# Kernel tuning notes

Measured on AMD Instinct MI355X. Metric: run time of the kernel, lower is better.

The kernel has to match this reference:

```python
import jax, jax.numpy as jnp
import numpy as np

ALPHA = 0.1       # args.alpha
T = 1.0           # args.T temperature
SIGMA = 64.0      # Gaussian kernel bandwidth of kernel_function
B_CONST = 1.0     # B in get_lambda
N_ITERS = 50      # 2^-50 << tol=1e-8, matches the break condition of the 1000-iter loop
HW = 256          # image resolution (upsample target)


def _features(feat):
    # get_feature: bilinear upsample (align_corners=False == half-pixel, as jax.image.resize) then sigmoid(x/T)
    n, c, _, _ = feat.shape
    up = jax.image.resize(feat, (n, c, HW, HW), method='bilinear')
    return jax.nn.sigmoid(up / T)


def setup_inputs() -> dict:
    key = jax.random.key(0)
    k1, k2, k3, k4 = jax.random.split(key, 4)
    return {
        'cal_feat': jax.random.normal(k1, (256, 1, 64, 64), jnp.float32),
        'test_feat': jax.random.normal(k2, (32, 1, 64, 64), jnp.float32),
        'cal_gt': jax.random.randint(k3, (256, 1, 256, 256), 0, 2, jnp.int32),
        'test_gt': jax.random.randint(k4, (32, 1, 256, 256), 0, 2, jnp.int32),
    }


def reference(cal_feat, test_feat, cal_gt, test_gt):
    cal_res = _features(cal_feat)    # [N,1,H,W] in (0,1)
    test_res = _features(test_feat)  # [B,1,H,W]
    N = cal_res.shape[0]
    B = test_res.shape[0]
    f32 = cal_res.dtype

    # kernel_function.get_weight: Gaussian RBF on flattened features, plus self-weight 1, row-normalized -> [B, N+1]
    cf = cal_res.reshape(N, -1)
    tf = test_res.reshape(B, -1)
    d2 = (tf * tf).sum(-1)[:, None] + (cf * cf).sum(-1)[None, :] - 2.0 * (tf @ cf.T)
    k = jnp.exp(-d2 / (2.0 * SIGMA * SIGMA))
    w = jnp.concatenate([k, jnp.ones((B, 1), f32)], axis=1)
    w = w / w.sum(axis=1, keepdims=True)

    # FNR_i(t) = #{positive pixels of cal sample i with score < t} / #positives
    # (pred = res >= t, so false negatives are positive pixels with res < t). Precompute sorted
    # positive-pixel scores per cal sample so the bisection is a batched searchsorted.
    gt = (cal_gt > 0).reshape(N, -1)
    pos = jnp.sum(gt, axis=1)                                    # [N]
    scores = jnp.where(gt, cal_res.reshape(N, -1), jnp.inf)
    sorted_scores = jnp.sort(scores, axis=1)                     # [N, HW*HW], padding at +inf
    pos_f = jnp.maximum(pos, 1).astype(f32)

    def fnr_at(t):  # t: [B] thresholds -> [N, B]
        cnt = jax.vmap(lambda s: jnp.searchsorted(s, t, side='left'))(sorted_scores)
        return cnt.astype(f32) / pos_f[:, None]

    # batched bisection on lambda (get_lambda, vectorized over the B test samples)
    def body(carry, _):
        low, high = carry
        lam = 0.5 * (low + high)
        fnr = fnr_at(1.0 - lam)                                   # [N, B]
        risk = jnp.einsum('bn,nb->b', w[:, :-1], fnr) + w[:, -1] * B_CONST
        high = jnp.where(risk < ALPHA, lam, high)
        low = jnp.where(risk >= ALPHA, lam, low)
        return (low, high), None

    init = (jnp.zeros((B,), f32), jnp.ones((B,), f32))
    (low, _), _ = jax.lax.scan(body, init, None, length=N_ITERS)
    lam = low  # _lambda = low after the loop

    # prediction set, size and per-test FNR (get_fnr_list on the test sample)
    pred = test_res >= (1.0 - lam)[:, None, None, None]           # [B,1,H,W] bool
    size = jnp.sum(pred, axis=(1, 2, 3)).astype(f32)
    tgt = test_gt > 0
    tp = jnp.sum(pred & tgt, axis=(1, 2, 3)).astype(f32)
    tpos = jnp.maximum(jnp.sum(tgt, axis=(1, 2, 3)), 1).astype(f32)
    fnr_test = 1.0 - tp / tpos                                    # fdr_tensor, [B]
    return fnr_test, lam, size
```

## Files before the change

kernel.cpp:

```cpp
#include <hip/hip_runtime.h>


#define NPIX 65536
#define HB 16256
#define CDF_STRIDE 16272
#define ALPHA 0.1f

#define OFF_TESTRES  0
#define OFF_CALBF    8388608u
#define OFF_TESTBF   41943040u
#define OFF_GROUPED  46137344u
#define OFF_CDF      79691776u
#define OFF_GPART    96354304u
#define OFF_CC       98451456u
#define OFF_TT       98452480u
#define OFF_THR      98452608u
#define OFF_LAM      98452736u
#define OFF_FACC     98452864u

typedef __attribute__((ext_vector_type(8))) short bf16x8;
typedef __attribute__((ext_vector_type(16))) float f32x16;

__device__ __forceinline__ unsigned short f2bf_rne(float f) {
  unsigned u = __float_as_uint(f);
  return (unsigned short)((u + 0x7FFFu + ((u >> 16) & 1u)) >> 16);
}

__device__ __forceinline__ int hsl(int b) { return b ^ ((b >> 6) & 31); }

__device__ __forceinline__ float score_at(const float* __restrict__ sfeat,
                                          int x0, int x1, float wx, int y) {
  float sy = 0.25f * (float)y - 0.375f;
  int y0 = (int)floorf(sy);
  float wy = sy - (float)y0;
  int y1 = y0 + 1;
  if (y0 < 0) y0 = 0;
  if (y1 > 63) y1 = 63;
  float a = sfeat[y0 * 64 + x0] * (1.f - wx) + sfeat[y0 * 64 + x1] * wx;
  float b = sfeat[y1 * 64 + x0] * (1.f - wx) + sfeat[y1 * 64 + x1] * wx;
  float v = a * (1.f - wy) + b * wy;
  return 1.f / (1.f + __expf(-v));
}

__global__ __launch_bounds__(1024, 4) void k_calt(const float* __restrict__ featc,
                                                  const int* __restrict__ gt,
                                                  unsigned short* __restrict__ calbf,
                                                  unsigned* __restrict__ cdf,
                                                  unsigned short* __restrict__ grouped,
                                                  float* __restrict__ cc,
                                                  const float* __restrict__ featt,
                                                  float* __restrict__ tres,
                                                  unsigned short* __restrict__ tbf) {
  __shared__ unsigned smem[16704];
  __shared__ float sfeat[4096];
  __shared__ float tfeat[4096];
  const int tid = threadIdx.x;
  const int lane = tid & 63, wv = tid >> 6;
  const int x = tid & 255, yq = tid >> 8;
  float sx = 0.25f * (float)x - 0.375f;
  int x0 = (int)floorf(sx);
  float wx = sx - (float)x0;
  int x1 = x0 + 1;
  if (x0 < 0) x0 = 0;
  if (x1 > 63) x1 = 63;

  const int n = blockIdx.x;
  const int b = n >> 3, sl = n & 7;
  for (int i = tid; i < HB; i += 1024) smem[i] = 0;
  for (int i = tid; i < 4096; i += 1024) {
    sfeat[i] = featc[n * 4096 + i];
    tfeat[i] = featt[b * 4096 + i];
  }
  const int* gtn = gt + (size_t)n * NPIX;
  unsigned short* cbn = calbf + (size_t)n * NPIX;
  __syncthreads();

  {
    float* resb = tres + (size_t)b * NPIX + sl * 8192;
    unsigned short* tbn = tbf + (size_t)b * NPIX + sl * 8192;
    #pragma unroll
    for (int i = 0; i < 8; ++i) {
      int y = sl * 32 + i * 4 + yq;
      float s = score_at(tfeat, x0, x1, wx, y);
      int q = i * 1024 + tid;
      resb[q] = s;
      tbn[q] = f2bf_rne(s);
    }
  }

  unsigned long long pm = 0ull;
  float sumsq = 0.f;
  #pragma unroll 4
  for (int it = 0; it < 64; ++it) {
    int y = it * 4 + yq;
    float s = score_at(sfeat, x0, x1, wx, y);
    int p = (y << 8) + x;
    unsigned short bh = f2bf_rne(s);
    cbn[p] = bh;
    float sr = __uint_as_float((unsigned)bh << 16);
    sumsq += sr * sr;
    if (gtn[p] > 0) {
      pm |= (1ull << it);
      atomicAdd(&smem[hsl((int)(__float_as_uint(s) >> 16))], 1u);
    }
  }
  #pragma unroll
  for (int off = 32; off; off >>= 1) sumsq += __shfl_xor(sumsq, off);
  if (lane == 0) smem[16272 + wv] = __float_as_uint(sumsq);
  __syncthreads();
  if (tid == 0) {
    float c = 0.f;
    for (int w = 0; w < 16; ++w) c += __uint_as_float(smem[16272 + w]);
    cc[n] = c;
  }
  unsigned* cdfn = cdf + (size_t)n * CDF_STRIDE;
  if (tid < 256) {
    const int base = tid * 64;
    unsigned psum = 0;
    if (base < HB) {
      for (int j = 0; j < 64; ++j) psum += smem[hsl(base + j)];
    }
    unsigned inc = psum;
    #pragma unroll
    for (int off = 1; off < 64; off <<= 1) {
      unsigned v = __shfl_up(inc, off);
      if (lane >= off) inc += v;
    }
    if (lane == 63) smem[16256 + wv] = inc;
    smem[16320 + tid] = inc - psum;
  }
  __syncthreads();
  if (tid < 256) {
    unsigned woff = 0;
    for (int w = 0; w < wv; ++w) woff += smem[16256 + w];
    unsigned run = woff + smem[16320 + tid];
    const int base = tid * 64;
    if (base < HB) {
      for (int j = 0; j < 64; ++j) {
        int sj = hsl(base + j);
        unsigned hcnt = smem[sj];
        cdfn[base + j] = run;
        smem[sj] = run;
        run += hcnt;
      }
    }
    if (tid == 0)
      cdfn[HB] = smem[16256] + smem[16257] + smem[16258] + smem[16259];
  }
  __syncthreads();
  unsigned short* gn = grouped + (size_t)n * NPIX;
  for (int it = 0; it < 64; ++it) {
    if (pm & (1ull << it)) {
      int y = it * 4 + yq;
      float s = score_at(sfeat, x0, x1, wx, y);
      unsigned bits = __float_as_uint(s);
      unsigned idx = atomicAdd(&smem[hsl((int)(bits >> 16))], 1u);
      gn[idx] = (unsigned short)(bits & 0xFFFFu);
    }
  }
}

__global__ __launch_bounds__(1024) void k_tt(const unsigned short* __restrict__ tbf,
                                             float* __restrict__ tt) {
  __shared__ unsigned smem[16];
  const int tid = threadIdx.x;
  const int lane = tid & 63, wv = tid >> 6;
  const int x = tid & 255, yq = tid >> 8;
  const int b = blockIdx.x;
  const unsigned short* tbn = tbf + (size_t)b * NPIX;
  float sumsq = 0.f;
  #pragma unroll 4
  for (int it = 0; it < 64; ++it) {
    int p = ((it * 4 + yq) << 8) + x;
    float sr = __uint_as_float((unsigned)tbn[p] << 16);
    sumsq += sr * sr;
  }
  #pragma unroll
  for (int off = 32; off; off >>= 1) sumsq += __shfl_xor(sumsq, off);
  if (lane == 0) smem[wv] = __float_as_uint(sumsq);
  __syncthreads();
  if (tid == 0) {
    float t = 0.f;
    for (int w = 0; w < 16; ++w) t += __uint_as_float(smem[w]);
    tt[b] = t;
  }
}

__global__ __launch_bounds__(256) void k_gemm(const unsigned short* __restrict__ tbf,
                                              const unsigned short* __restrict__ cbf,
                                              float* __restrict__ gpart) {
  __shared__ __align__(16) unsigned short As[16384];
  __shared__ __align__(16) unsigned short Bs[16384];
  __shared__ float lred[4][1024];
  const int tid = threadIdx.x;
  const int lane = tid & 63, wv = tid >> 6;
  const int r = lane & 31, half = lane >> 5;
  const int nt = blockIdx.x;
  f32x16 acc;
  #pragma unroll
  for (int i = 0; i < 16; ++i) acc[i] = 0.f;
  for (int ch = 0; ch < 2; ++ch) {
    const size_t kbase = (size_t)blockIdx.y * 1024 + ch * 512;
    __syncthreads();
    #pragma unroll
    for (int s = 0; s < 16; ++s) {
      int flat = s * 256 + tid;
      int rem = flat & 2047;
      int row = rem >> 6, kb = rem & 63;
      const unsigned short* src = (flat >= 2048)
          ? cbf + (size_t)(nt * 32 + row) * NPIX + kbase + kb * 8
          : tbf + (size_t)row * NPIX + kbase + kb * 8;
      int slot = ((kb << 5) + row) ^ (kb & 31);
      int4 v = *(const int4*)src;
      *(int4*)((flat >= 2048 ? Bs : As) + slot * 8) = v;
    }
    __syncthreads();
    #pragma unroll
    for (int i = 0; i < 8; ++i) {
      int k8 = (wv << 4) + i * 2 + half;
      int slot = ((k8 << 5) + r) ^ (k8 & 31);
      bf16x8 a = *(const bf16x8*)(As + slot * 8);
      bf16x8 b = *(const bf16x8*)(Bs + slot * 8);
      acc = __builtin_amdgcn_mfma_f32_32x32x16_bf16(a, b, acc, 0, 0, 0);
    }
  }
  #pragma unroll
  for (int rg = 0; rg < 16; ++rg) {
    int m = (rg & 3) + 8 * (rg >> 2) + 4 * half;
    lred[wv][m * 32 + r] = acc[rg];
  }
  __syncthreads();
  float* gp = gpart + (size_t)(blockIdx.y * 8 + nt) * 1024;
  for (int e = tid; e < 1024; e += 256)
    gp[e] = lred[0][e] + lred[1][e] + lred[2][e] + lred[3][e];
}

__global__ __launch_bounds__(512) void k_quant(const float* __restrict__ gpart,
                                               const float* __restrict__ cc,
                                               const float* __restrict__ tt,
                                               const unsigned* __restrict__ cdf,
                                               const unsigned short* __restrict__ grouped,
                                               float* __restrict__ lam,
                                               float* __restrict__ thr,
                                               int* __restrict__ facc) {
  __shared__ float qs[256];
  __shared__ float bins[4096];
  __shared__ float red[8];
  __shared__ float bc[2];
  __shared__ unsigned sBin;
  const int b = blockIdx.x, tid = threadIdx.x;
  const int lane = tid & 63, wv = tid >> 6;

  if (tid < 4) facc[b * 4 + tid] = 0;
  for (int i = tid; i < 4096; i += 512) bins[i] = 0.f;
  if (tid == 0) sBin = 0xFFFFFFFFu;

  float k = 0.f;
  if (tid < 256) {
    const float* gp = gpart + ((tid >> 5) * 1024) + (b * 32) + (tid & 31);
    float g = 0.f;
    #pragma unroll 8
    for (int ks = 0; ks < 64; ++ks) g += gp[(size_t)ks * 8192];
    float d2 = tt[b] + cc[tid] - 2.f * g;
    k = expf(-d2 * (1.f / 8192.f));
  }
  float v = k;
  #pragma unroll
  for (int off = 32; off; off >>= 1) v += __shfl_xor(v, off);
  if (lane == 0) red[wv] = v;
  __syncthreads();
  if (tid == 0) {
    float ws = 1.f;
    for (int w = 0; w < 8; ++w) ws += red[w];
    bc[0] = ws;
  }
  __syncthreads();
  const float wsum = bc[0];
  const float wlast = 1.f / wsum;
  const float R = ALPHA - wlast;
  if (R <= 0.f) {
    if (tid == 0) { lam[b] = 1.0f; thr[b] = 0.0f; }
    return;
  }
  if (tid < 256) {
    unsigned pos = cdf[(size_t)tid * CDF_STRIDE + HB];
    qs[tid] = k / (wsum * (float)(pos ? pos : 1u));
  }
  __syncthreads();

  int lo = 0, hi = HB;
  float baseS = 0.f;
  for (int it = 0; it < 14; ++it) {
    int mid = (lo + hi) >> 1;
    float p = 0.f;
    if (tid < 256) p = qs[tid] * (float)cdf[(size_t)tid * CDF_STRIDE + mid];
    float r = p;
    #pragma unroll
    for (int off = 32; off; off >>= 1) r += __shfl_xor(r, off);
    if (lane == 0) red[wv] = r;
    __syncthreads();
    if (tid == 0) {
      float s = 0.f;
      for (int w = 0; w < 8; ++w) s += red[w];
      bc[1] = s;
    }
    __syncthreads();
    float S = bc[1];
    if (S < R) { lo = mid; baseS = S; } else { hi = mid; }
  }
  const int B = lo;

  {
    const int n = tid >> 1;
    const float q = qs[n];
    const unsigned* cn = cdf + (size_t)n * CDF_STRIDE;
    const unsigned short* gn = grouped + (size_t)n * NPIX;
    unsigned e0 = cn[B + 1];
    for (unsigned j = cn[B] + (tid & 1); j < e0; j += 2)
      atomicAdd(&bins[gn[j] >> 4], q);
  }
  __syncthreads();

  if (wv == 0) {
    float s = 0.f;
    for (int j = 0; j < 64; ++j) s += bins[lane * 64 + j];
    float inc = s;
    #pragma unroll
    for (int off = 1; off < 64; off <<= 1) {
      float u = __shfl_up(inc, off);
      if (lane >= off) inc += u;
    }
    float pre = inc - s;
    bool hit = (baseS + pre < R) && (baseS + inc >= R);
    unsigned long long m = __ballot(hit);
    int ow = m ? (__ffsll((unsigned long long)m) - 1) : -1;
    if (lane == ow) {
      float run = baseS + pre;
      unsigned bin = (unsigned)lane * 64 + 63;
      for (int j = 0; j < 64; ++j) {
        float bv = bins[lane * 64 + j];
        if (run + bv >= R) { bin = (unsigned)lane * 64 + j; break; }
        run += bv;
      }
      sBin = bin;
    }
    if (m == 0 && lane == 0) sBin = 4095u;
  }
  __syncthreads();
  if (tid == 0) {
    unsigned tb = ((unsigned)B << 16) | (sBin << 4);
    lam[b] = 1.0f - __uint_as_float(tb | 0x8u);
    thr[b] = __uint_as_float((tb | 0xFu) + 1u);
  }
}

__global__ __launch_bounds__(256) void k_finalp(const float* __restrict__ tres,
                                                const int* __restrict__ tgt,
                                                const float* __restrict__ thr,
                                                int* __restrict__ facc) {
  __shared__ int red[12];
  const int b = blockIdx.x, seg = blockIdx.y, tid = threadIdx.x;
  const int lane = tid & 63, wv = tid >> 6;
  const float th = thr[b];
  const float* rb = tres + (size_t)b * NPIX + seg * 8192;
  const int* gb = tgt + (size_t)b * NPIX + seg * 8192;
  int sz = 0, tp = 0, tpos = 0;
  for (int i = 0; i < 32; ++i) {
    int p = i * 256 + tid;
    int pred = (rb[p] >= th) ? 1 : 0;
    int tg = (gb[p] > 0) ? 1 : 0;
    sz += pred;
    tp += pred & tg;
    tpos += tg;
  }
  #pragma unroll
  for (int off = 32; off; off >>= 1) {
    sz += __shfl_xor(sz, off);
    tp += __shfl_xor(tp, off);
    tpos += __shfl_xor(tpos, off);
  }
  if (lane == 0) { red[wv] = sz; red[4 + wv] = tp; red[8 + wv] = tpos; }
  __syncthreads();
  if (tid == 0) {
    int s0 = red[0] + red[1] + red[2] + red[3];
    int s1 = red[4] + red[5] + red[6] + red[7];
    int s2 = red[8] + red[9] + red[10] + red[11];
    atomicAdd(&facc[b * 4 + 0], s0);
    atomicAdd(&facc[b * 4 + 1], s1);
    atomicAdd(&facc[b * 4 + 2], s2);
  }
}

__global__ void k_out(const int* __restrict__ facc, const float* __restrict__ lam,
                      float* __restrict__ out) {
  int b = threadIdx.x;
  if (b < 32) {
    int sz = facc[b * 4], tp = facc[b * 4 + 1], tpos = facc[b * 4 + 2];
    float tposf = (float)(tpos > 0 ? tpos : 1);
    out[b] = 1.f - (float)tp / tposf;
    out[32 + b] = lam[b];
    out[64 + b] = (float)sz;
  }
}

extern "C" void kernel_launch(void* const* d_in, const int* in_sizes, int n_in,
                              void* d_out, int out_size, void* d_ws, size_t ws_size,
                              hipStream_t stream) {
  const float* cal_feat = (const float*)d_in[0];
  const float* test_feat = (const float*)d_in[1];
  const int* cal_gt = (const int*)d_in[2];
  const int* test_gt = (const int*)d_in[3];
  float* out = (float*)d_out;
  char* ws = (char*)d_ws;

  float* test_res = (float*)(ws + OFF_TESTRES);
  unsigned short* cal_bf = (unsigned short*)(ws + OFF_CALBF);
  unsigned short* test_bf = (unsigned short*)(ws + OFF_TESTBF);
  unsigned short* grouped = (unsigned short*)(ws + OFF_GROUPED);
  unsigned* cdf = (unsigned*)(ws + OFF_CDF);
  float* gpart = (float*)(ws + OFF_GPART);
  float* cc = (float*)(ws + OFF_CC);
  float* tt = (float*)(ws + OFF_TT);
  float* thr = (float*)(ws + OFF_THR);
  float* lam = (float*)(ws + OFF_LAM);
  int* facc = (int*)(ws + OFF_FACC);

  k_calt<<<dim3(256), dim3(1024), 0, stream>>>(cal_feat, cal_gt, cal_bf, cdf, grouped, cc,
                                               test_feat, test_res, test_bf);
  k_tt<<<dim3(32), dim3(1024), 0, stream>>>(test_bf, tt);
  k_gemm<<<dim3(8, 64), dim3(256), 0, stream>>>(test_bf, cal_bf, gpart);
  k_quant<<<dim3(32), dim3(512), 0, stream>>>(gpart, cc, tt, cdf, grouped, lam, thr, facc);
  k_finalp<<<dim3(32, 8), dim3(256), 0, stream>>>(test_res, test_gt, thr, facc);
  k_out<<<dim3(1), dim3(64), 0, stream>>>(facc, lam, out);
}
```

Measured before the change: 255.3 us.

## Pack histogram into 16-bit pairs, stage grouped scatter in LDS, vectorize final pass

Packs two adjacent 16-bit histogram bins into each 32-bit LDS word, halving histogram memory. The prefix scan now uses all 1024 threads instead of 256. The freed LDS holds a staging buffer, so the bucketed scatter of positive scores goes to shared memory and is then written to global memory contiguously instead of as random global stores. The final prediction kernel reads float4/int4 vectors. The trade-off is much higher LDS use per block (launch bound drops from 4 to 2 blocks), and 16-bit packed counts could overflow if a bin pair ever exceeds 65535.

```diff
diff --git a/kernel.cpp b/kernel.cpp
--- a/kernel.cpp
+++ b/kernel.cpp
@@ -5,6 +5,7 @@
 #define HB 16256
 #define CDF_STRIDE 16272
 #define ALPHA 0.1f
+#define STAGE_CAP 40960
 
 #define OFF_TESTRES  0
 #define OFF_CALBF    8388608u
@@ -26,7 +27,7 @@
   return (unsigned short)((u + 0x7FFFu + ((u >> 16) & 1u)) >> 16);
 }
 
-__device__ __forceinline__ int hsl(int b) { return b ^ ((b >> 6) & 31); }
+__device__ __forceinline__ int SW(int w) { return w ^ ((w >> 5) & 31); }
 
 __device__ __forceinline__ float score_at(const float* __restrict__ sfeat,
                                           int x0, int x1, float wx, int y) {
@@ -42,7 +43,7 @@
   return 1.f / (1.f + __expf(-v));
 }
 
-__global__ __launch_bounds__(1024, 4) void k_calt(const float* __restrict__ featc,
+__global__ __launch_bounds__(1024, 2) void k_calt(const float* __restrict__ featc,
                                                   const int* __restrict__ gt,
                                                   unsigned short* __restrict__ calbf,
                                                   unsigned* __restrict__ cdf,
@@ -51,9 +52,10 @@
                                                   const float* __restrict__ featt,
                                                   float* __restrict__ tres,
                                                   unsigned short* __restrict__ tbf) {
-  __shared__ unsigned smem[16704];
+  __shared__ unsigned smem[9264];
   __shared__ float sfeat[4096];
   __shared__ float tfeat[4096];
+  __shared__ unsigned short sstage[STAGE_CAP];
   const int tid = threadIdx.x;
   const int lane = tid & 63, wv = tid >> 6;
   const int x = tid & 255, yq = tid >> 8;
@@ -66,7 +68,7 @@
 
   const int n = blockIdx.x;
   const int b = n >> 3, sl = n & 7;
-  for (int i = tid; i < HB; i += 1024) smem[i] = 0;
+  for (int i = tid; i < 8192; i += 1024) smem[i] = 0;
   for (int i = tid; i < 4096; i += 1024) {
     sfeat[i] = featc[n * 4096 + i];
     tfeat[i] = featt[b * 4096 + i];
@@ -90,7 +92,7 @@
 
   unsigned long long pm = 0ull;
   float sumsq = 0.f;
-  #pragma unroll 4
+  #pragma unroll 8
   for (int it = 0; it < 64; ++it) {
     int y = it * 4 + yq;
     float s = score_at(sfeat, x0, x1, wx, y);
@@ -101,52 +103,59 @@
     sumsq += sr * sr;
     if (gtn[p] > 0) {
       pm |= (1ull << it);
-      atomicAdd(&smem[hsl((int)(__float_as_uint(s) >> 16))], 1u);
+      unsigned bits = __float_as_uint(s);
+      atomicAdd(&smem[SW((int)(bits >> 17))], (bits & 0x10000u) ? 0x10000u : 1u);
     }
   }
   #pragma unroll
   for (int off = 32; off; off >>= 1) sumsq += __shfl_xor(sumsq, off);
-  if (lane == 0) smem[16272 + wv] = __float_as_uint(sumsq);
+  if (lane == 0) smem[8208 + wv] = __float_as_uint(sumsq);
   __syncthreads();
   if (tid == 0) {
     float c = 0.f;
-    for (int w = 0; w < 16; ++w) c += __uint_as_float(smem[16272 + w]);
+    for (int w = 0; w < 16; ++w) c += __uint_as_float(smem[8208 + w]);
     cc[n] = c;
   }
+  const int wbase = tid * 8;
+  unsigned psum = 0;
+  #pragma unroll
+  for (int j = 0; j < 8; ++j) {
+    unsigned w = smem[SW(wbase + j)];
+    psum += (w & 0xFFFFu) + (w >> 16);
+  }
+  unsigned inc = psum;
+  #pragma unroll
+  for (int off = 1; off < 64; off <<= 1) {
+    unsigned v = __shfl_up(inc, off);
+    if (lane >= off) inc += v;
+  }
+  if (lane == 63) smem[8192 + wv] = inc;
+  smem[8224 + tid] = inc - psum;
+  __syncthreads();
+  {
+    unsigned woff = 0;
+    for (int w = 0; w < wv; ++w) woff += smem[8192 + w];
+    unsigned run = woff + smem[8224 + tid];
+    #pragma unroll
+    for (int j = 0; j < 8; ++j) {
+      int si = SW(wbase + j);
+      unsigned w = smem[si];
+      unsigned clo = run;
+      run += (w & 0xFFFFu);
+      unsigned chi = run;
+      run += (w >> 16);
+      smem[si] = (chi << 16) | clo;
+    }
+    if (tid == 1023) smem[9248] = run;
+  }
+  __syncthreads();
   unsigned* cdfn = cdf + (size_t)n * CDF_STRIDE;
-  if (tid < 256) {
-    const int base = tid * 64;
-    unsigned psum = 0;
-    if (base < HB) {
-      for (int j = 0; j < 64; ++j) psum += smem[hsl(base + j)];
-    }
-    unsigned inc = psum;
-    #pragma unroll
-    for (int off = 1; off < 64; off <<= 1) {
-      unsigned v = __shfl_up(inc, off);
-      if (lane >= off) inc += v;
-    }
-    if (lane == 63) smem[16256 + wv] = inc;
-    smem[16320 + tid] = inc - psum;
-  }
-  __syncthreads();
-  if (tid < 256) {
-    unsigned woff = 0;
-    for (int w = 0; w < wv; ++w) woff += smem[16256 + w];
-    unsigned run = woff + smem[16320 + tid];
-    const int base = tid * 64;
-    if (base < HB) {
-      for (int j = 0; j < 64; ++j) {
-        int sj = hsl(base + j);
-        unsigned hcnt = smem[sj];
-        cdfn[base + j] = run;
-        smem[sj] = run;
-        run += hcnt;
-      }
-    }
-    if (tid == 0)
-      cdfn[HB] = smem[16256] + smem[16257] + smem[16258] + smem[16259];
-  }
+  for (int i = tid; i < HB; i += 1024) {
+    unsigned w = smem[SW(i >> 1)];
+    cdfn[i] = (i & 1) ? (w >> 16) : (w & 0xFFFFu);
+  }
+  const unsigned pos = smem[9248];
+  if (tid == 0) cdfn[HB] = pos;
   __syncthreads();
   unsigned short* gn = grouped + (size_t)n * NPIX;
   for (int it = 0; it < 64; ++it) {
@@ -154,10 +163,16 @@
       int y = it * 4 + yq;
       float s = score_at(sfeat, x0, x1, wx, y);
       unsigned bits = __float_as_uint(s);
-      unsigned idx = atomicAdd(&smem[hsl((int)(bits >> 16))], 1u);
-      gn[idx] = (unsigned short)(bits & 0xFFFFu);
-    }
-  }
+      unsigned old = atomicAdd(&smem[SW((int)(bits >> 17))], (bits & 0x10000u) ? 0x10000u : 1u);
+      unsigned idx = (bits & 0x10000u) ? (old >> 16) : (old & 0xFFFFu);
+      unsigned short lo = (unsigned short)(bits & 0xFFFFu);
+      if (idx < STAGE_CAP) sstage[idx] = lo;
+      else gn[idx] = lo;
+    }
+  }
+  __syncthreads();
+  unsigned lim = pos < STAGE_CAP ? pos : STAGE_CAP;
+  for (unsigned i = tid; i < lim; i += 1024) gn[i] = sstage[i];
 }
 
 __global__ __launch_bounds__(1024) void k_tt(const unsigned short* __restrict__ tbf,
@@ -362,16 +377,20 @@
   const int b = blockIdx.x, seg = blockIdx.y, tid = threadIdx.x;
   const int lane = tid & 63, wv = tid >> 6;
   const float th = thr[b];
-  const float* rb = tres + (size_t)b * NPIX + seg * 8192;
-  const int* gb = tgt + (size_t)b * NPIX + seg * 8192;
+  const float4* rb4 = (const float4*)(tres + (size_t)b * NPIX + seg * 8192);
+  const int4* gb4 = (const int4*)(tgt + (size_t)b * NPIX + seg * 8192);
   int sz = 0, tp = 0, tpos = 0;
-  for (int i = 0; i < 32; ++i) {
-    int p = i * 256 + tid;
-    int pred = (rb[p] >= th) ? 1 : 0;
-    int tg = (gb[p] > 0) ? 1 : 0;
-    sz += pred;
-    tp += pred & tg;
-    tpos += tg;
+  #pragma unroll
+  for (int i = 0; i < 8; ++i) {
+    float4 r4 = rb4[i * 256 + tid];
+    int4 g4 = gb4[i * 256 + tid];
+    int p0 = (r4.x >= th), t0 = (g4.x > 0);
+    int p1 = (r4.y >= th), t1 = (g4.y > 0);
+    int p2 = (r4.z >= th), t2 = (g4.z > 0);
+    int p3 = (r4.w >= th), t3 = (g4.w > 0);
+    sz += p0 + p1 + p2 + p3;
+    tp += (p0 & t0) + (p1 & t1) + (p2 & t2) + (p3 & t3);
+    tpos += t0 + t1 + t2 + t3;
   }
   #pragma unroll
   for (int off = 32; off; off >>= 1) {
```

Result: faster. 246.9 us (-3.3%).
